# Kernel tuning notes

Measured on AMD Instinct MI355X. Metric: run time of the kernel, lower is better.

Reference implementation:

```python
import jax, jax.numpy as jnp
import numpy as np

N, D, DIM, H = 50000, 32, 128, 4  # nodes, fixed degree, feature dim, heads


def setup_inputs() -> dict:
    key = jax.random.key(0)
    ks = jax.random.split(key, 8)
    s = 1.0 / np.sqrt(DIM)
    h = jax.random.normal(ks[0], (N, DIM), dtype=jnp.float32)
    neigh_idx = jax.random.randint(ks[1], (N, D), 0, N, dtype=jnp.int32)
    W = jax.random.uniform(ks[2], (H, DIM, DIM), jnp.float32, -s, s)   # per-head fciandj
    a1 = jax.random.uniform(ks[3], (H, DIM), jnp.float32, -s, s)       # key weight, src half
    a2 = jax.random.uniform(ks[4], (H, DIM), jnp.float32, -s, s)       # key weight, nbr half
    Wg = jax.random.uniform(ks[5], (DIM, H), jnp.float32, -s, s)       # GetGate projection
    W0 = jax.random.uniform(ks[6], (H * DIM, DIM), jnp.float32, -s, s) # output mix w0
    return {"h": h, "neigh_idx": neigh_idx, "W": W, "a1": a1, "a2": a2, "Wg": Wg, "W0": W0}


def reference(h, neigh_idx, W, a1, a2, Wg, W0):
    # gate per node per head (GetGate assumed: softmax over heads of linear proj)
    g = jax.nn.softmax(h @ Wg, axis=-1)            # [N, H]
    hjs = h[neigh_idx]                              # [N, D, d] per-edge gather (shared across heads)
    heads = []
    for k in range(W.shape[0]):
        wh = h @ W[k]                               # [N, d]
        whjs = jnp.einsum('ndi,ij->ndj', hjs, W[k]) # [N, D, d]
        # edge score: key([wh_i, wh_j]) = wh_i.a1 + wh_j.a2, then leaky_relu
        e = jax.nn.leaky_relu((wh @ a1[k])[:, None] + whjs @ a2[k])  # [N, D]
        att = jax.nn.softmax(e, axis=1)             # segment softmax over neighbors
        out = jax.nn.relu(jnp.einsum('nd,ndj->nj', att, whjs))       # [N, d]
        heads.append(g[:, k:k + 1] * out)
    return jnp.concatenate(heads, axis=-1) @ W0     # [N, d]
```

## Files before the change

kernel.cpp:

```cpp
#include <hip/hip_runtime.h>

typedef __attribute__((ext_vector_type(8))) short short8;
typedef __attribute__((ext_vector_type(4))) float f32x4;

__device__ __forceinline__ float bf2f(unsigned u16) {
    union { float f; unsigned u32; } v; v.u32 = u16 << 16; return v.f;
}
__device__ __forceinline__ unsigned short f2bf(float f) {
    union { float f; unsigned u32; } v; v.f = f;
    unsigned x = v.u32;
    x += ((x >> 16) & 1u) + 0x7FFFu;
    return (unsigned short)(x >> 16);
}
__device__ __forceinline__ unsigned packbf(float a, float b) {
    return (unsigned)f2bf(a) | ((unsigned)f2bf(b) << 16);
}

__global__ __launch_bounds__(256) void kb12(const float* __restrict__ W,
                                            const float* __restrict__ a1,
                                            const float* __restrict__ a2,
                                            float* __restrict__ b1,
                                            float* __restrict__ b2) {
    const int t = threadIdx.x;
    const int grp = blockIdx.x * 16 + (t >> 4);
    const int q = t & 15;
    const int k = grp >> 7, i = grp & 127;

    const float* wr = &W[k * 16384 + i * 128 + q * 8];
    const float* A1 = &a1[k * 128 + q * 8];
    const float* A2 = &a2[k * 128 + q * 8];
    float4 w0 = *(const float4*)wr;
    float4 w1 = *(const float4*)(wr + 4);
    float4 x0 = *(const float4*)A1;
    float4 x1 = *(const float4*)(A1 + 4);
    float4 y0 = *(const float4*)A2;
    float4 y1 = *(const float4*)(A2 + 4);
    float v1 = w0.x*x0.x + w0.y*x0.y + w0.z*x0.z + w0.w*x0.w
             + w1.x*x1.x + w1.y*x1.y + w1.z*x1.z + w1.w*x1.w;
    float v2 = w0.x*y0.x + w0.y*y0.y + w0.z*y0.z + w0.w*y0.w
             + w1.x*y1.x + w1.y*y1.y + w1.z*y1.z + w1.w*y1.w;
    #pragma unroll
    for (int m = 8; m >= 1; m >>= 1) {
        v1 += __shfl_xor(v1, m, 16);
        v2 += __shfl_xor(v2, m, 16);
    }
    if (q == 0) { b1[k * 128 + i] = v1; b2[k * 128 + i] = v2; }
}

__global__ __launch_bounds__(256) void kscore(const float* __restrict__ h,
                                              const float* __restrict__ Wg,
                                              const float* __restrict__ b1,
                                              const float* __restrict__ b2,
                                              const float* __restrict__ W,
                                              const float* __restrict__ W0,
                                              unsigned* __restrict__ hb32,
                                              float* __restrict__ s1,
                                              float* __restrict__ s2,
                                              float* __restrict__ g,
                                              unsigned short* __restrict__ Wt,
                                              unsigned short* __restrict__ W0t,
                                              int N) {
    const int b = blockIdx.x, t = threadIdx.x;
    if (b < 256) {
        #pragma unroll
        for (int e = 0; e < 2; ++e) {
            int i = b * 512 + e * 256 + t;
            if (i < 65536) {
                int head = i >> 14, rem = i & 16383, k = rem >> 7, col = rem & 127;
                Wt[head * 16384 + col * 128 + k] = f2bf(W[i]);
            } else {
                int i2 = i - 65536;
                int k = i2 >> 7, col = i2 & 127;
                W0t[col * 512 + k] = f2bf(W0[i2]);
            }
        }
        return;
    }
    const int w = t >> 6, l = t & 63;
    const int grp = l >> 4, q = l & 15;
    const int n = (b - 256) * 16 + w * 4 + grp;
    if (n >= N) return;

    float4 hv0 = *(const float4*)&h[(size_t)n * 128 + q * 8];
    float4 hv1 = *(const float4*)&h[(size_t)n * 128 + q * 8 + 4];
    float ha[8] = {hv0.x, hv0.y, hv0.z, hv0.w, hv1.x, hv1.y, hv1.z, hv1.w};

    uint4 hbv;
    hbv.x = packbf(ha[0], ha[1]); hbv.y = packbf(ha[2], ha[3]);
    hbv.z = packbf(ha[4], ha[5]); hbv.w = packbf(ha[6], ha[7]);
    *(uint4*)&hb32[(size_t)n * 64 + q * 4] = hbv;

    float p[12];
    #pragma unroll
    for (int k = 0; k < 4; ++k) {
        float4 ba = *(const float4*)&b1[k * 128 + q * 8];
        float4 bb = *(const float4*)&b1[k * 128 + q * 8 + 4];
        p[k] = ha[0]*ba.x + ha[1]*ba.y + ha[2]*ba.z + ha[3]*ba.w
             + ha[4]*bb.x + ha[5]*bb.y + ha[6]*bb.z + ha[7]*bb.w;
        float4 ca = *(const float4*)&b2[k * 128 + q * 8];
        float4 cb = *(const float4*)&b2[k * 128 + q * 8 + 4];
        p[4+k] = ha[0]*ca.x + ha[1]*ca.y + ha[2]*ca.z + ha[3]*ca.w
               + ha[4]*cb.x + ha[5]*cb.y + ha[6]*cb.z + ha[7]*cb.w;
    }
    p[8] = p[9] = p[10] = p[11] = 0.f;
    #pragma unroll
    for (int e = 0; e < 8; ++e) {
        float4 wg = *(const float4*)&Wg[(q * 8 + e) * 4];
        p[8]  += ha[e] * wg.x;
        p[9]  += ha[e] * wg.y;
        p[10] += ha[e] * wg.z;
        p[11] += ha[e] * wg.w;
    }
    #pragma unroll
    for (int m = 8; m >= 1; m >>= 1) {
        #pragma unroll
        for (int i = 0; i < 12; ++i) p[i] += __shfl_xor(p[i], m, 16);
    }
    if (q == 0) {
        *(float4*)&s1[n * 4] = make_float4(p[0], p[1], p[2], p[3]);
        *(float4*)&s2[n * 4] = make_float4(p[4], p[5], p[6], p[7]);
        float mx = fmaxf(fmaxf(p[8], p[9]), fmaxf(p[10], p[11]));
        float e0 = __expf(p[8] - mx), e1 = __expf(p[9] - mx);
        float e2 = __expf(p[10] - mx), e3 = __expf(p[11] - mx);
        float si = 1.f / (e0 + e1 + e2 + e3);
        *(float4*)&g[n * 4] = make_float4(e0 * si, e1 * si, e2 * si, e3 * si);
    }
}

__global__ __launch_bounds__(256) void k3_mix(const int* __restrict__ idx,
                                              const unsigned* __restrict__ hb32,
                                              const float* __restrict__ s1,
                                              const float* __restrict__ s2,
                                              unsigned* __restrict__ Mx32,
                                              int N) {
    __shared__ float att4s[4][32][4];
    const int t = threadIdx.x, w = t >> 6, l = t & 63;
    const int d = l & 31, half = l >> 5;
    int n = blockIdx.x * 4 + w;
    const bool valid = (n < N);
    if (!valid) n = N - 1;

    int j = idx[(size_t)n * 32 + d];
    float2 s2v = *(const float2*)&s2[(size_t)j * 4 + half * 2];
    const float* s1p = &s1[(size_t)n * 4];
    float e0 = s1p[half * 2] + s2v.x;
    float e1 = s1p[half * 2 + 1] + s2v.y;
    e0 = (e0 >= 0.f) ? e0 : 0.01f * e0;
    e1 = (e1 >= 0.f) ? e1 : 0.01f * e1;
    float m0 = e0, m1 = e1;
    #pragma unroll
    for (int mm = 16; mm >= 1; mm >>= 1) {
        m0 = fmaxf(m0, __shfl_xor(m0, mm, 32));
        m1 = fmaxf(m1, __shfl_xor(m1, mm, 32));
    }
    float p0 = __expf(e0 - m0), p1 = __expf(e1 - m1);
    float q0 = p0, q1 = p1;
    #pragma unroll
    for (int mm = 16; mm >= 1; mm >>= 1) {
        q0 += __shfl_xor(q0, mm, 32);
        q1 += __shfl_xor(q1, mm, 32);
    }
    *(float2*)&att4s[w][d][half * 2] = make_float2(p0 / q0, p1 / q1);

    float ac[4][2] = {};
    #pragma unroll
    for (int dd = 0; dd < 32; ++dd) {
        int jj = __shfl(j, dd, 64);
        unsigned hv = hb32[(size_t)jj * 64 + l];
        float h0 = bf2f(hv & 0xffffu);
        float h1 = bf2f(hv >> 16);
        float4 a4 = *(const float4*)&att4s[w][dd][0];
        ac[0][0] += a4.x * h0; ac[0][1] += a4.x * h1;
        ac[1][0] += a4.y * h0; ac[1][1] += a4.y * h1;
        ac[2][0] += a4.z * h0; ac[2][1] += a4.z * h1;
        ac[3][0] += a4.w * h0; ac[3][1] += a4.w * h1;
    }
    if (valid) {
        #pragma unroll
        for (int k = 0; k < 4; ++k)
            Mx32[(size_t)n * 256 + k * 64 + l] = packbf(ac[k][0], ac[k][1]);
    }
}

typedef const __attribute__((address_space(1))) char gbyte;
typedef __attribute__((address_space(3))) char lbyte;

__global__ __launch_bounds__(512, 2) void k4_gemm(const unsigned short* __restrict__ Mx,
                                                  const unsigned short* __restrict__ Wt,
                                                  const unsigned short* __restrict__ W0t,
                                                  const float* __restrict__ g,
                                                  float* __restrict__ out,
                                                  int N, int T) {
    __shared__ unsigned short Uin[32 * 512];
    __shared__ unsigned short Uout[32 * 512];
    __shared__ float gld[128];
    const int tid = threadIdx.x, w = tid >> 6, l = tid & 63;
    const int l15 = l & 15, lh = l >> 4;
    const int hd = w & 3, ch = w >> 2;
    const int P = gridDim.x;

    short8 bf1[4][4];
    #pragma unroll
    for (int s = 0; s < 4; ++s)
        #pragma unroll
        for (int c = 0; c < 4; ++c)
            bf1[s][c] = *(const short8*)&Wt[(size_t)hd * 16384 +
                                            (size_t)((ch * 4 + c) * 16 + l15) * 128 + s * 32 + lh * 8];
    short8 bf2[16];
    #pragma unroll
    for (int ks = 0; ks < 16; ++ks)
        bf2[ks] = *(const short8*)&W0t[(size_t)(w * 16 + l15) * 512 + ks * 32 + lh * 8];

    const int t0 = blockIdx.x;

    auto STAGE = [&](int tile) {
        const size_t n0 = (size_t)tile * 32;
        if (w == 0 && l < 32) {
            size_t n = n0 + l; if (n >= (size_t)N) n = N - 1;
            __builtin_amdgcn_global_load_lds((gbyte*)((const char*)g + n * 16),
                                             (lbyte*)&gld[0], 16, 0, 0);
        }
        #pragma unroll
        for (int p = 0; p < 4; ++p) {
            int r = p * 8 + w;
            size_t n = n0 + r;
            if (n >= (size_t)N) n = N - 1;
            const char* src = (const char*)Mx + n * 1024 + ((l * 16) ^ ((r & 7) << 4));
            __builtin_amdgcn_global_load_lds((gbyte*)src, (lbyte*)&Uin[r * 512], 16, 0, 0);
        }
    };

    STAGE(t0);
    __syncthreads();

    for (int t = t0; t < T; t += P) {
        const int n0 = t * 32;

        const char* Uib = (const char*)Uin;
        #pragma unroll
        for (int rg = 0; rg < 2; ++rg) {
            const int arow = rg * 16 + l15;
            short8 af[4];
            #pragma unroll
            for (int s = 0; s < 4; ++s) {
                int ab = arow * 1024 + hd * 256 + s * 64 + lh * 16;
                af[s] = *(const short8*)(Uib + (ab ^ ((arow & 7) << 4)));
            }
            f32x4 acc[4] = {};
            #pragma unroll
            for (int s = 0; s < 4; ++s)
                #pragma unroll
                for (int c = 0; c < 4; ++c)
                    acc[c] = __builtin_amdgcn_mfma_f32_16x16x32_bf16(af[s], bf1[s][c], acc[c], 0, 0, 0);
            #pragma unroll
            for (int c = 0; c < 4; ++c) {
                const int col = hd * 128 + (ch * 4 + c) * 16 + l15;
                #pragma unroll
                for (int r = 0; r < 4; ++r) {
                    int row = rg * 16 + lh * 4 + r;
                    float v = fmaxf(acc[c][r], 0.f) * gld[row * 4 + hd];
                    int ub = row * 1024 + col * 2;
                    *(unsigned short*)((char*)Uout + (ub ^ ((row & 7) << 4))) = f2bf(v);
                }
            }
        }

        __syncthreads();

        if (t + P < T) STAGE(t + P);

        const char* Uob = (const char*)Uout;
        #pragma unroll
        for (int rg = 0; rg < 2; ++rg) {
            const int arow = rg * 16 + l15;
            f32x4 oaccA = {}, oaccB = {};
            #pragma unroll
            for (int ks = 0; ks < 16; ks += 2) {
                int abA = arow * 1024 + ks * 64 + lh * 16;
                int abB = abA + 64;
                short8 afrA = *(const short8*)(Uob + (abA ^ ((arow & 7) << 4)));
                short8 afrB = *(const short8*)(Uob + (abB ^ ((arow & 7) << 4)));
                oaccA = __builtin_amdgcn_mfma_f32_16x16x32_bf16(afrA, bf2[ks], oaccA, 0, 0, 0);
                oaccB = __builtin_amdgcn_mfma_f32_16x16x32_bf16(afrB, bf2[ks + 1], oaccB, 0, 0, 0);
            }
            f32x4 oacc = oaccA + oaccB;
            #pragma unroll
            for (int r = 0; r < 4; ++r) {
                int n = n0 + rg * 16 + lh * 4 + r;
                if (n < N) out[(size_t)n * 128 + w * 16 + l15] = oacc[r];
            }
        }

        __syncthreads();
    }
}

extern "C" void kernel_launch(void* const* d_in, const int* in_sizes, int n_in,
                              void* d_out, int out_size, void* d_ws, size_t ws_size,
                              hipStream_t stream) {
    const float* h     = (const float*)d_in[0];
    const int*   neigh = (const int*)d_in[1];
    const float* W     = (const float*)d_in[2];
    const float* a1    = (const float*)d_in[3];
    const float* a2    = (const float*)d_in[4];
    const float* Wg    = (const float*)d_in[5];
    const float* W0    = (const float*)d_in[6];
    float* out = (float*)d_out;

    const int N = in_sizes[0] / 128;

    char* ws = (char*)d_ws;
    unsigned* hb32 = (unsigned*)ws;
    unsigned* Mx32 = (unsigned*)(ws + (size_t)N * 256);
    float* s1 = (float*)(ws + (size_t)N * 256 + (size_t)N * 1024);
    float* s2 = s1 + (size_t)N * 4;
    float* g  = s2 + (size_t)N * 4;
    unsigned short* Wt  = (unsigned short*)(g + (size_t)N * 4);
    unsigned short* W0t = Wt + 65536;
    float* b1 = (float*)(W0t + 65536);
    float* b2 = b1 + 512;

    const int T = (N + 31) / 32;
    const int P = (T < 256) ? T : 256;

    kb12<<<dim3(32), dim3(256), 0, stream>>>(W, a1, a2, b1, b2);
    kscore<<<dim3((N + 15) / 16 + 256), dim3(256), 0, stream>>>(h, Wg, b1, b2, W, W0,
                                                                hb32, s1, s2, g, Wt, W0t, N);
    k3_mix<<<dim3((N + 3) / 4), dim3(256), 0, stream>>>(neigh, hb32, s1, s2, Mx32, N);
    k4_gemm<<<dim3(P), dim3(512), 0, stream>>>((const unsigned short*)Mx32, Wt, W0t, g,
                                               out, N, T);
}
```

Before: 118.0 us.

## Replace persistent LDS-staged GEMM with one-tile-per-block direct-load kernel

The persistent 512-thread GEMM kernel, which kept weights in registers and prefetched Mx tiles into LDS through global_load_lds, is replaced by a non-persistent 256-thread kernel that handles one 32-row tile per block. A-fragments come straight from global memory, gate values are loaded into registers, and the Wt/W0t fragments are reloaded per block in two halves. This removes the LDS input buffer and the loop barriers and raises block count for occupancy. The cost is that every block re-reads the full weight matrices, which adds global/L2 traffic in place of the amortized register-resident weights.

```diff
diff --git a/kernel.cpp b/kernel.cpp
--- a/kernel.cpp
+++ b/kernel.cpp
@@ -182,70 +182,43 @@
     }
 }
 
-typedef const __attribute__((address_space(1))) char gbyte;
-typedef __attribute__((address_space(3))) char lbyte;
-
-__global__ __launch_bounds__(512, 2) void k4_gemm(const unsigned short* __restrict__ Mx,
-                                                  const unsigned short* __restrict__ Wt,
-                                                  const unsigned short* __restrict__ W0t,
-                                                  const float* __restrict__ g,
-                                                  float* __restrict__ out,
-                                                  int N, int T) {
-    __shared__ unsigned short Uin[32 * 512];
+__global__ __launch_bounds__(256) void k4_direct(const unsigned short* __restrict__ Mx,
+                                                 const unsigned short* __restrict__ Wt,
+                                                 const unsigned short* __restrict__ W0t,
+                                                 const float* __restrict__ g,
+                                                 float* __restrict__ out,
+                                                 int N) {
     __shared__ unsigned short Uout[32 * 512];
-    __shared__ float gld[128];
     const int tid = threadIdx.x, w = tid >> 6, l = tid & 63;
     const int l15 = l & 15, lh = l >> 4;
-    const int hd = w & 3, ch = w >> 2;
-    const int P = gridDim.x;
-
-    short8 bf1[4][4];
-    #pragma unroll
-    for (int s = 0; s < 4; ++s)
-        #pragma unroll
-        for (int c = 0; c < 4; ++c)
-            bf1[s][c] = *(const short8*)&Wt[(size_t)hd * 16384 +
-                                            (size_t)((ch * 4 + c) * 16 + l15) * 128 + s * 32 + lh * 8];
-    short8 bf2[16];
-    #pragma unroll
-    for (int ks = 0; ks < 16; ++ks)
-        bf2[ks] = *(const short8*)&W0t[(size_t)(w * 16 + l15) * 512 + ks * 32 + lh * 8];
-
-    const int t0 = blockIdx.x;
-
-    auto STAGE = [&](int tile) {
-        const size_t n0 = (size_t)tile * 32;
-        if (w == 0 && l < 32) {
-            size_t n = n0 + l; if (n >= (size_t)N) n = N - 1;
-            __builtin_amdgcn_global_load_lds((gbyte*)((const char*)g + n * 16),
-                                             (lbyte*)&gld[0], 16, 0, 0);
+    const int n0 = blockIdx.x * 32;
+
+    float gv[2][4];
+    #pragma unroll
+    for (int rg = 0; rg < 2; ++rg)
+        #pragma unroll
+        for (int r = 0; r < 4; ++r) {
+            int n = n0 + rg * 16 + lh * 4 + r;
+            gv[rg][r] = (n < N) ? g[(size_t)n * 4 + w] : 0.f;
         }
-        #pragma unroll
-        for (int p = 0; p < 4; ++p) {
-            int r = p * 8 + w;
-            size_t n = n0 + r;
-            if (n >= (size_t)N) n = N - 1;
-            const char* src = (const char*)Mx + n * 1024 + ((l * 16) ^ ((r & 7) << 4));
-            __builtin_amdgcn_global_load_lds((gbyte*)src, (lbyte*)&Uin[r * 512], 16, 0, 0);
-        }
-    };
-
-    STAGE(t0);
-    __syncthreads();
-
-    for (int t = t0; t < T; t += P) {
-        const int n0 = t * 32;
-
-        const char* Uib = (const char*)Uin;
+
+    #pragma unroll
+    for (int chalf = 0; chalf < 2; ++chalf) {
+        short8 bf1[4][4];
+        #pragma unroll
+        for (int s = 0; s < 4; ++s)
+            #pragma unroll
+            for (int c = 0; c < 4; ++c)
+                bf1[s][c] = *(const short8*)&Wt[(size_t)w * 16384 +
+                                 (size_t)((chalf * 4 + c) * 16 + l15) * 128 + s * 32 + lh * 8];
         #pragma unroll
         for (int rg = 0; rg < 2; ++rg) {
-            const int arow = rg * 16 + l15;
+            int arow = n0 + rg * 16 + l15;
+            if (arow >= N) arow = N - 1;
             short8 af[4];
             #pragma unroll
-            for (int s = 0; s < 4; ++s) {
-                int ab = arow * 1024 + hd * 256 + s * 64 + lh * 16;
-                af[s] = *(const short8*)(Uib + (ab ^ ((arow & 7) << 4)));
-            }
+            for (int s = 0; s < 4; ++s)
+                af[s] = *(const short8*)&Mx[(size_t)arow * 512 + w * 128 + s * 32 + lh * 8];
             f32x4 acc[4] = {};
             #pragma unroll
             for (int s = 0; s < 4; ++s)
@@ -254,22 +227,27 @@
                     acc[c] = __builtin_amdgcn_mfma_f32_16x16x32_bf16(af[s], bf1[s][c], acc[c], 0, 0, 0);
             #pragma unroll
             for (int c = 0; c < 4; ++c) {
-                const int col = hd * 128 + (ch * 4 + c) * 16 + l15;
+                const int col = w * 128 + (chalf * 4 + c) * 16 + l15;
                 #pragma unroll
                 for (int r = 0; r < 4; ++r) {
                     int row = rg * 16 + lh * 4 + r;
-                    float v = fmaxf(acc[c][r], 0.f) * gld[row * 4 + hd];
+                    float v = fmaxf(acc[c][r], 0.f) * gv[rg][r];
                     int ub = row * 1024 + col * 2;
                     *(unsigned short*)((char*)Uout + (ub ^ ((row & 7) << 4))) = f2bf(v);
                 }
             }
         }
-
-        __syncthreads();
-
-        if (t + P < T) STAGE(t + P);
-
-        const char* Uob = (const char*)Uout;
+    }
+    __syncthreads();
+
+    const char* Uob = (const char*)Uout;
+    #pragma unroll
+    for (int c2 = 0; c2 < 2; ++c2) {
+        const int cg = w * 2 + c2;
+        short8 bf2[16];
+        #pragma unroll
+        for (int ks = 0; ks < 16; ++ks)
+            bf2[ks] = *(const short8*)&W0t[(size_t)(cg * 16 + l15) * 512 + ks * 32 + lh * 8];
         #pragma unroll
         for (int rg = 0; rg < 2; ++rg) {
             const int arow = rg * 16 + l15;
@@ -287,11 +265,9 @@
             #pragma unroll
             for (int r = 0; r < 4; ++r) {
                 int n = n0 + rg * 16 + lh * 4 + r;
-                if (n < N) out[(size_t)n * 128 + w * 16 + l15] = oacc[r];
+                if (n < N) out[(size_t)n * 128 + cg * 16 + l15] = oacc[r];
             }
         }
-
-        __syncthreads();
     }
 }
 
@@ -320,13 +296,10 @@
     float* b1 = (float*)(W0t + 65536);
     float* b2 = b1 + 512;
 
-    const int T = (N + 31) / 32;
-    const int P = (T < 256) ? T : 256;
-
     kb12<<<dim3(32), dim3(256), 0, stream>>>(W, a1, a2, b1, b2);
     kscore<<<dim3((N + 15) / 16 + 256), dim3(256), 0, stream>>>(h, Wg, b1, b2, W, W0,
                                                                 hb32, s1, s2, g, Wt, W0t, N);
     k3_mix<<<dim3((N + 3) / 4), dim3(256), 0, stream>>>(neigh, hb32, s1, s2, Mx32, N);
-    k4_gemm<<<dim3(P), dim3(512), 0, stream>>>((const unsigned short*)Mx32, Wt, W0t, g,
-                                               out, N, T);
-}
+    k4_direct<<<dim3((N + 31) / 32), dim3(256), 0, stream>>>((const unsigned short*)Mx32,
+                                                             Wt, W0t, g, out, N);
+}
```

After: 155.9 us. +32.1%, slower.
